# Kernel tuning notes

Measured on AMD Instinct MI355X. Metric: run time of the kernel, lower is better.

## Reference

```python
import jax, jax.numpy as jnp
import numpy as np

G, K, P = 200000, 32, 2048
TOP_K = 5
MIN_DIST = 0.1
EPS = 1e-8


def setup_inputs() -> dict:
    key = jax.random.key(0)
    k1, k2, k3, k4, k5 = jax.random.split(key, 5)
    A_logits = jax.random.normal(k1, (G, K), dtype=jnp.float32) * 0.01
    x = jax.random.normal(k2, (G, 3), dtype=jnp.float32)
    weights = jax.random.uniform(k3, (G,), dtype=jnp.float32)
    # scale so pred_mask = sum_g R[p,g] ~ 0.5 (rows of softmax(A) sum to 1)
    R = jax.random.uniform(k4, (P, G), dtype=jnp.float32) * (1.0 / G)
    instance_mask = jax.random.randint(k5, (P,), 0, 2, dtype=jnp.int32)
    return {"A_logits": A_logits, "x": x, "weights": weights, "R": R,
            "instance_mask": instance_mask}


def _total_loss(A_logits, x, weights, R, instance_mask):
    A = jax.nn.softmax(A_logits, axis=1)  # (G, K)

    # --- render mask loss (BCE on clamped soft mask) ---
    r_pc = R @ A                                   # (P, K)
    pred = jnp.clip(r_pc.sum(axis=1), 0.0, 1.0)    # (P,)
    t = instance_mask.astype(jnp.float32)
    log_p = jnp.maximum(jnp.log(pred), -100.0)     # torch BCE clamps log at -100
    log_1mp = jnp.maximum(jnp.log1p(-pred), -100.0)
    render = -jnp.mean(t * log_p + (1.0 - t) * log_1mp)

    # --- cluster stats + dispersion loss ---
    Aw = A * weights[:, None]                      # (G, K)
    occupancy = Aw.sum(axis=0) + EPS               # (K,)
    centroids = (Aw.T @ x) / occupancy[:, None]    # (K, 3)
    diff = x[None, :, :] - centroids[:, None, :]   # (K, G, 3)
    sq_dist = (diff ** 2).sum(-1)                  # (K, G)
    dispersion = (sq_dist * Aw.T).sum(axis=1) / occupancy  # (K,)
    disp = dispersion.sum()

    # --- separation loss: sum_{i<j} relu(min_dist - ||c_i - c_j||)^2 ---
    d = jnp.linalg.norm(centroids[:, None, :] - centroids[None, :, :], axis=-1)  # (K, K)
    pen = jax.nn.relu(MIN_DIST - d) ** 2
    sep = jnp.sum(jnp.triu(pen, k=1))

    # --- covisibility loss: per-gaussian pairwise sq-diffs of top-k probs ---
    # sum_{i<j} (v_i - v_j)^2 = k * sum v_i^2 - (sum v_i)^2
    top_vals, _ = jax.lax.top_k(A, TOP_K)          # (G, TOP_K)
    pair = TOP_K * (top_vals ** 2).sum(axis=1) - top_vals.sum(axis=1) ** 2
    cov = pair.mean()

    # --- prune loss ---
    prune = jnp.abs(weights).sum()

    return render + disp + sep + cov + prune


def reference(A_logits, x, weights, R, instance_mask):
    return _total_loss(A_logits, x, weights, R, instance_mask)
```

## Files before the change

kernel.cpp:

```cpp
#include <hip/hip_runtime.h>

#define G_N 200000
#define K_N 32
#define P_N 2048
#define EPSV 1e-8f
#define MINDIST 0.1f

#define PA_BLOCKS ((G_N + 255) / 256)
#define TOTAL_BLOCKS (P_N + PA_BLOCKS)

__device__ __forceinline__ float wave_reduce_sum(float v) {
#pragma unroll
  for (int d = 1; d < 64; d <<= 1) v += __shfl_xor(v, d, 64);
  return v;
}

__global__ __launch_bounds__(256) void fused_main(
    const float* __restrict__ A, const float* __restrict__ x,
    const float* __restrict__ wts, const float* __restrict__ R,
    float* __restrict__ pred_sum, float* __restrict__ acc)
{
  __shared__ float smem[164];
  const int tid  = threadIdx.x;
  const int lane = tid & 63;
  const int wid  = tid >> 6;

  if (blockIdx.x < P_N) {
    const int p = blockIdx.x;
    const float4* row = (const float4*)(R + (size_t)p * G_N);
    float s0 = 0.f, s1 = 0.f;
    int i = tid;
    for (; i + 256 < (G_N / 4); i += 512) {
      float4 v0 = row[i];
      float4 v1 = row[i + 256];
      s0 += (v0.x + v0.y) + (v0.z + v0.w);
      s1 += (v1.x + v1.y) + (v1.z + v1.w);
    }
    for (; i < (G_N / 4); i += 256) {
      float4 v = row[i];
      s0 += (v.x + v.y) + (v.z + v.w);
    }
    float s = wave_reduce_sum(s0 + s1);
    if (lane == 0) smem[wid] = s;
    __syncthreads();
    if (tid == 0) pred_sum[p] = (smem[0] + smem[1]) + (smem[2] + smem[3]);
    return;
  }

  const int g = (blockIdx.x - P_N) * 256 + tid;
  for (int i = tid; i < 162; i += 256) smem[i] = 0.f;
  __syncthreads();

  float p[K_N];
  float covp = 0.f, prw = 0.f;
  float wg = 0.f, x0 = 0.f, x1 = 0.f, x2 = 0.f, q = 0.f;

  if (g < G_N) {
    const float4* Ar = (const float4*)(A + (size_t)g * K_N);
    float a[K_N];
#pragma unroll
    for (int j = 0; j < 8; j++) {
      float4 v = Ar[j];
      a[4 * j + 0] = v.x; a[4 * j + 1] = v.y;
      a[4 * j + 2] = v.z; a[4 * j + 3] = v.w;
    }
    float m = a[0];
#pragma unroll
    for (int k = 1; k < K_N; k++) m = fmaxf(m, a[k]);
    float s = 0.f;
#pragma unroll
    for (int k = 0; k < K_N; k++) { p[k] = __expf(a[k] - m); s += p[k]; }
    const float invs = 1.f / s;

    float t0 = 0.f, t1 = 0.f, t2 = 0.f, t3 = 0.f, t4 = 0.f;
#pragma unroll
    for (int k = 0; k < K_N; k++) {
      p[k] *= invs;
      float v = p[k], mx;
      mx = fmaxf(t0, v); v = fminf(t0, v); t0 = mx;
      mx = fmaxf(t1, v); v = fminf(t1, v); t1 = mx;
      mx = fmaxf(t2, v); v = fminf(t2, v); t2 = mx;
      mx = fmaxf(t3, v); v = fminf(t3, v); t3 = mx;
      mx = fmaxf(t4, v); v = fminf(t4, v); t4 = mx;
    }
    float d01 = t0 - t1, d02 = t0 - t2, d03 = t0 - t3, d04 = t0 - t4;
    float d12 = t1 - t2, d13 = t1 - t3, d14 = t1 - t4;
    float d23 = t2 - t3, d24 = t2 - t4, d34 = t3 - t4;
    covp = d01*d01 + d02*d02 + d03*d03 + d04*d04 + d12*d12
         + d13*d13 + d14*d14 + d23*d23 + d24*d24 + d34*d34;

    wg = wts[g];
    prw = fabsf(wg);
    x0 = x[3 * g + 0]; x1 = x[3 * g + 1]; x2 = x[3 * g + 2];
    q = x0 * x0 + x1 * x1 + x2 * x2;
  } else {
#pragma unroll
    for (int k = 0; k < K_N; k++) p[k] = 0.f;
  }

#pragma unroll
  for (int k = 0; k < K_N; k++) {
    float c = wg * p[k];
    float v0 = c, v1 = c * x0, v2 = c * x1, v3 = c * x2, v4 = c * q;
#pragma unroll
    for (int d = 1; d < 64; d <<= 1) {
      v0 += __shfl_xor(v0, d, 64);
      v1 += __shfl_xor(v1, d, 64);
      v2 += __shfl_xor(v2, d, 64);
      v3 += __shfl_xor(v3, d, 64);
      v4 += __shfl_xor(v4, d, 64);
    }
    if (lane == 0) {
      atomicAdd(&smem[k],       v0);
      atomicAdd(&smem[32 + k],  v1);
      atomicAdd(&smem[64 + k],  v2);
      atomicAdd(&smem[96 + k],  v3);
      atomicAdd(&smem[128 + k], v4);
    }
  }
  covp = wave_reduce_sum(covp);
  prw  = wave_reduce_sum(prw);
  if (lane == 0) {
    atomicAdd(&smem[160], covp);
    atomicAdd(&smem[161], prw);
  }
  __syncthreads();
  if (tid < 162) atomicAdd(&acc[tid], smem[tid]);
}

__global__ __launch_bounds__(256) void finalize_k(
    const float* __restrict__ pred_sum, const int* __restrict__ mask,
    const float* __restrict__ acc, float* __restrict__ out)
{
  __shared__ float sred[4];
  __shared__ float cent[K_N][3];
  const int tid  = threadIdx.x;
  const int lane = tid & 63;
  const int wid  = tid >> 6;

  float bce = 0.f;
  for (int i = tid; i < P_N; i += 256) {
    float pred = fminf(fmaxf(pred_sum[i], 0.f), 1.f);
    float t = (float)mask[i];
    float lp = fmaxf(logf(pred), -100.f);
    float l1 = fmaxf(log1pf(-pred), -100.f);
    bce += t * lp + (1.f - t) * l1;
  }
  bce = wave_reduce_sum(bce);
  if (lane == 0) sred[wid] = bce;
  __syncthreads();
  const float render = -((sred[0] + sred[1]) + (sred[2] + sred[3])) / (float)P_N;

  float disp_v = 0.f, sep_v = 0.f;
  if (tid < K_N) {
    float W  = acc[tid];
    float Sx = acc[32 + tid], Sy = acc[64 + tid], Sz = acc[96 + tid];
    float Q  = acc[128 + tid];
    float occ = W + EPSV;
    float inv = 1.f / occ;
    float cx = Sx * inv, cy = Sy * inv, cz = Sz * inv;
    cent[tid][0] = cx; cent[tid][1] = cy; cent[tid][2] = cz;
    disp_v = (Q - 2.f * (cx * Sx + cy * Sy + cz * Sz)
              + (cx * cx + cy * cy + cz * cz) * W) * inv;
  }
  __syncthreads();

  if (tid < K_N) {
    for (int j = tid + 1; j < K_N; j++) {
      float dx = cent[tid][0] - cent[j][0];
      float dy = cent[tid][1] - cent[j][1];
      float dz = cent[tid][2] - cent[j][2];
      float d = sqrtf(dx * dx + dy * dy + dz * dz);
      float r = fmaxf(MINDIST - d, 0.f);
      sep_v += r * r;
    }
  }
  if (tid < 64) {
    float dsum = wave_reduce_sum(disp_v);
    float ssum = wave_reduce_sum(sep_v);
    if (tid == 0) {
      float cov   = acc[160] / (float)G_N;
      float prune = acc[161];
      out[0] = render + dsum + ssum + cov + prune;
    }
  }
}

extern "C" void kernel_launch(void* const* d_in, const int* in_sizes, int n_in,
                              void* d_out, int out_size, void* d_ws, size_t ws_size,
                              hipStream_t stream) {
  const float* A    = (const float*)d_in[0];
  const float* x    = (const float*)d_in[1];
  const float* wts  = (const float*)d_in[2];
  const float* R    = (const float*)d_in[3];
  const int*   mask = (const int*)d_in[4];
  float* out = (float*)d_out;

  float* ws       = (float*)d_ws;
  float* pred_sum = ws;
  float* acc      = ws + P_N;

  hipMemsetAsync(acc, 0, 162 * sizeof(float), stream);
  fused_main<<<TOTAL_BLOCKS, 256, 0, stream>>>(A, x, wts, R, pred_sum, acc);
  finalize_k<<<1, 256, 0, stream>>>(pred_sum, mask, acc, out);
}
```

Before: 326.3 us.

## Restructure into persistent blocks with dynamic R streaming and LDS-based cluster stats

Replaces the launch of one block per R row plus one block per 256 gaussians with 512 persistent blocks. In each block, one wave computes cluster statistics for a contiguous gaussian range by staging weighted probabilities in LDS and accumulating per-cluster sums, which replaces the 160 shuffle reductions per wave. All waves in the block pull 512-float4 chunks of four R rows from an LDS work counter, so the gaussian work overlaps the R streaming. This is meant to cut the shuffle-reduction cost and to balance the bandwidth-bound R read. The price is heavier global atomics (per-lane adds into acc from every block) and per-lane row-boundary tracking.

```diff
diff --git a/kernel.cpp b/kernel.cpp
--- a/kernel.cpp
+++ b/kernel.cpp
@@ -6,8 +6,12 @@
 #define EPSV 1e-8f
 #define MINDIST 0.1f
 
-#define PA_BLOCKS ((G_N + 255) / 256)
-#define TOTAL_BLOCKS (P_N + PA_BLOCKS)
+#define NBLK 512
+#define ROWS_PER_BLK 4
+#define ROW_F4 (G_N / 4)
+#define REG_F4 (ROWS_PER_BLK * ROW_F4)
+#define GRAB_F4 512
+#define NGRABS ((REG_F4 + GRAB_F4 - 1) / GRAB_F4)
 
 __device__ __forceinline__ float wave_reduce_sum(float v) {
 #pragma unroll
@@ -20,112 +24,138 @@
     const float* __restrict__ wts, const float* __restrict__ R,
     float* __restrict__ pred_sum, float* __restrict__ acc)
 {
-  __shared__ float smem[164];
+  __shared__ float pw[64 * 36];
+  __shared__ float4 xq[64];
+  __shared__ float rowacc[ROWS_PER_BLK];
+  __shared__ int ctr;
+
   const int tid  = threadIdx.x;
   const int lane = tid & 63;
-  const int wid  = tid >> 6;
-
-  if (blockIdx.x < P_N) {
-    const int p = blockIdx.x;
-    const float4* row = (const float4*)(R + (size_t)p * G_N);
-    float s0 = 0.f, s1 = 0.f;
-    int i = tid;
-    for (; i + 256 < (G_N / 4); i += 512) {
-      float4 v0 = row[i];
-      float4 v1 = row[i + 256];
-      s0 += (v0.x + v0.y) + (v0.z + v0.w);
-      s1 += (v1.x + v1.y) + (v1.z + v1.w);
-    }
-    for (; i < (G_N / 4); i += 256) {
-      float4 v = row[i];
-      s0 += (v.x + v.y) + (v.z + v.w);
-    }
-    float s = wave_reduce_sum(s0 + s1);
-    if (lane == 0) smem[wid] = s;
-    __syncthreads();
-    if (tid == 0) pred_sum[p] = (smem[0] + smem[1]) + (smem[2] + smem[3]);
-    return;
-  }
-
-  const int g = (blockIdx.x - P_N) * 256 + tid;
-  for (int i = tid; i < 162; i += 256) smem[i] = 0.f;
-  __syncthreads();
-
-  float p[K_N];
-  float covp = 0.f, prw = 0.f;
-  float wg = 0.f, x0 = 0.f, x1 = 0.f, x2 = 0.f, q = 0.f;
-
-  if (g < G_N) {
-    const float4* Ar = (const float4*)(A + (size_t)g * K_N);
-    float a[K_N];
+  const int b    = blockIdx.x;
+
+  if (tid < ROWS_PER_BLK) rowacc[tid] = 0.f;
+  if (tid == 0) ctr = 0;
+  __syncthreads();
+
+  if (tid < 64) {
+    const int gstart = (int)(((long long)b * G_N) / NBLK);
+    const int gend   = (int)(((long long)(b + 1) * G_N) / NBLK);
+    const int h = lane >> 5, k = lane & 31;
+    float cW = 0.f, cX = 0.f, cY = 0.f, cZ = 0.f, cQ = 0.f;
+    float covp = 0.f, prw = 0.f;
+
+    for (int g0 = gstart; g0 < gend; g0 += 64) {
+      const int g = g0 + lane;
+      float av[K_N];
+      float4 xv = make_float4(0.f, 0.f, 0.f, 0.f);
+      if (g < gend) {
+        const float4* Ar = (const float4*)(A + (size_t)g * K_N);
+#pragma unroll
+        for (int j = 0; j < 8; j++) {
+          float4 v = Ar[j];
+          av[4*j+0] = v.x; av[4*j+1] = v.y; av[4*j+2] = v.z; av[4*j+3] = v.w;
+        }
+        float m = av[0];
+#pragma unroll
+        for (int kk = 1; kk < K_N; kk++) m = fmaxf(m, av[kk]);
+        float s = 0.f;
+#pragma unroll
+        for (int kk = 0; kk < K_N; kk++) { av[kk] = __expf(av[kk] - m); s += av[kk]; }
+        const float invs = 1.f / s;
+
+        float t0 = 0.f, t1 = 0.f, t2 = 0.f, t3 = 0.f, t4 = 0.f;
+#pragma unroll
+        for (int kk = 0; kk < K_N; kk++) {
+          float v = av[kk], mx;
+          mx = fmaxf(t0, v); v = fminf(t0, v); t0 = mx;
+          mx = fmaxf(t1, v); v = fminf(t1, v); t1 = mx;
+          mx = fmaxf(t2, v); v = fminf(t2, v); t2 = mx;
+          mx = fmaxf(t3, v); v = fminf(t3, v); t3 = mx;
+          mx = fmaxf(t4, v); v = fminf(t4, v); t4 = mx;
+        }
+        t0 *= invs; t1 *= invs; t2 *= invs; t3 *= invs; t4 *= invs;
+        float d01 = t0-t1, d02 = t0-t2, d03 = t0-t3, d04 = t0-t4;
+        float d12 = t1-t2, d13 = t1-t3, d14 = t1-t4;
+        float d23 = t2-t3, d24 = t2-t4, d34 = t3-t4;
+        covp += d01*d01 + d02*d02 + d03*d03 + d04*d04 + d12*d12
+              + d13*d13 + d14*d14 + d23*d23 + d24*d24 + d34*d34;
+
+        const float wg = wts[g];
+        prw += fabsf(wg);
+        const float x0 = x[3*g+0], x1 = x[3*g+1], x2 = x[3*g+2];
+        xv = make_float4(x0, x1, x2, x0*x0 + x1*x1 + x2*x2);
+        const float cw = wg * invs;
+#pragma unroll
+        for (int kk = 0; kk < K_N; kk++) av[kk] *= cw;
+      } else {
+#pragma unroll
+        for (int kk = 0; kk < K_N; kk++) av[kk] = 0.f;
+      }
+
+#pragma unroll
+      for (int j = 0; j < 8; j++)
+        *(float4*)&pw[lane * 36 + 4*j] =
+            make_float4(av[4*j+0], av[4*j+1], av[4*j+2], av[4*j+3]);
+      xq[lane] = xv;
+
+#pragma unroll
+      for (int i = 0; i < 32; i++) {
+        const float c = pw[(h*32 + i) * 36 + k];
+        const float4 xg = xq[h*32 + i];
+        cW += c; cX += c*xg.x; cY += c*xg.y; cZ += c*xg.z; cQ += c*xg.w;
+      }
+    }
+
+    cW += __shfl_xor(cW, 32, 64); cX += __shfl_xor(cX, 32, 64);
+    cY += __shfl_xor(cY, 32, 64); cZ += __shfl_xor(cZ, 32, 64);
+    cQ += __shfl_xor(cQ, 32, 64);
+    covp = wave_reduce_sum(covp);
+    prw  = wave_reduce_sum(prw);
+    if (lane < 32) {
+      atomicAdd(&acc[       k], cW);
+      atomicAdd(&acc[ 32  + k], cX);
+      atomicAdd(&acc[ 64  + k], cY);
+      atomicAdd(&acc[ 96  + k], cZ);
+      atomicAdd(&acc[128  + k], cQ);
+    }
+    if (lane == 0) { atomicAdd(&acc[160], covp); atomicAdd(&acc[161], prw); }
+  }
+
+  const float4* reg = (const float4*)R + (size_t)b * REG_F4;
+  int cur_row = 0, nb = ROW_F4;
+  float racc = 0.f;
+
+  for (;;) {
+    int grab;
+    if (lane == 0) grab = atomicAdd(&ctr, 1);
+    grab = __shfl(grab, 0, 64);
+    if (grab >= NGRABS) break;
+    const int base = grab * GRAB_F4;
+    const int nvalid = min(8, (REG_F4 - base) >> 6);
+
+    float4 v[8];
+#pragma unroll
+    for (int j = 0; j < 8; j++)
+      if (j < nvalid) v[j] = reg[base + j*64 + lane];
+
 #pragma unroll
     for (int j = 0; j < 8; j++) {
-      float4 v = Ar[j];
-      a[4 * j + 0] = v.x; a[4 * j + 1] = v.y;
-      a[4 * j + 2] = v.z; a[4 * j + 3] = v.w;
-    }
-    float m = a[0];
-#pragma unroll
-    for (int k = 1; k < K_N; k++) m = fmaxf(m, a[k]);
-    float s = 0.f;
-#pragma unroll
-    for (int k = 0; k < K_N; k++) { p[k] = __expf(a[k] - m); s += p[k]; }
-    const float invs = 1.f / s;
-
-    float t0 = 0.f, t1 = 0.f, t2 = 0.f, t3 = 0.f, t4 = 0.f;
-#pragma unroll
-    for (int k = 0; k < K_N; k++) {
-      p[k] *= invs;
-      float v = p[k], mx;
-      mx = fmaxf(t0, v); v = fminf(t0, v); t0 = mx;
-      mx = fmaxf(t1, v); v = fminf(t1, v); t1 = mx;
-      mx = fmaxf(t2, v); v = fminf(t2, v); t2 = mx;
-      mx = fmaxf(t3, v); v = fminf(t3, v); t3 = mx;
-      mx = fmaxf(t4, v); v = fminf(t4, v); t4 = mx;
-    }
-    float d01 = t0 - t1, d02 = t0 - t2, d03 = t0 - t3, d04 = t0 - t4;
-    float d12 = t1 - t2, d13 = t1 - t3, d14 = t1 - t4;
-    float d23 = t2 - t3, d24 = t2 - t4, d34 = t3 - t4;
-    covp = d01*d01 + d02*d02 + d03*d03 + d04*d04 + d12*d12
-         + d13*d13 + d14*d14 + d23*d23 + d24*d24 + d34*d34;
-
-    wg = wts[g];
-    prw = fabsf(wg);
-    x0 = x[3 * g + 0]; x1 = x[3 * g + 1]; x2 = x[3 * g + 2];
-    q = x0 * x0 + x1 * x1 + x2 * x2;
-  } else {
-#pragma unroll
-    for (int k = 0; k < K_N; k++) p[k] = 0.f;
-  }
-
-#pragma unroll
-  for (int k = 0; k < K_N; k++) {
-    float c = wg * p[k];
-    float v0 = c, v1 = c * x0, v2 = c * x1, v3 = c * x2, v4 = c * q;
-#pragma unroll
-    for (int d = 1; d < 64; d <<= 1) {
-      v0 += __shfl_xor(v0, d, 64);
-      v1 += __shfl_xor(v1, d, 64);
-      v2 += __shfl_xor(v2, d, 64);
-      v3 += __shfl_xor(v3, d, 64);
-      v4 += __shfl_xor(v4, d, 64);
-    }
-    if (lane == 0) {
-      atomicAdd(&smem[k],       v0);
-      atomicAdd(&smem[32 + k],  v1);
-      atomicAdd(&smem[64 + k],  v2);
-      atomicAdd(&smem[96 + k],  v3);
-      atomicAdd(&smem[128 + k], v4);
-    }
-  }
-  covp = wave_reduce_sum(covp);
-  prw  = wave_reduce_sum(prw);
-  if (lane == 0) {
-    atomicAdd(&smem[160], covp);
-    atomicAdd(&smem[161], prw);
-  }
-  __syncthreads();
-  if (tid < 162) atomicAdd(&acc[tid], smem[tid]);
+      if (j < nvalid) {
+        const int q = base + j*64 + lane;
+        if (q >= nb) {
+          atomicAdd(&rowacc[cur_row], racc);
+          cur_row = q / ROW_F4;
+          nb = (cur_row + 1) * ROW_F4;
+          racc = 0.f;
+        }
+        racc += (v[j].x + v[j].y) + (v[j].z + v[j].w);
+      }
+    }
+  }
+  atomicAdd(&rowacc[cur_row], racc);
+  __syncthreads();
+  if (tid < ROWS_PER_BLK)
+    pred_sum[b * ROWS_PER_BLK + tid] = rowacc[tid];
 }
 
 __global__ __launch_bounds__(256) void finalize_k(
@@ -201,6 +231,6 @@
   float* acc      = ws + P_N;
 
   hipMemsetAsync(acc, 0, 162 * sizeof(float), stream);
-  fused_main<<<TOTAL_BLOCKS, 256, 0, stream>>>(A, x, wts, R, pred_sum, acc);
+  fused_main<<<NBLK, 256, 0, stream>>>(A, x, wts, R, pred_sum, acc);
   finalize_k<<<1, 256, 0, stream>>>(pred_sum, mask, acc, out);
 }
```

Result: faster. 306.5 us (-6.1%).
